# Performance work log

Hardware: AMD Instinct MI355X
Metric: run time of the kernel (lower is better)

The kernel has to match this reference:

```python
import jax, jax.numpy as jnp
import numpy as np

N_NODES = 100000
N_EDGES = 1600000
D_IN = 128
D_OUT = 128


def setup_inputs() -> dict:
    key = jax.random.key(0)
    k1, k2, k3, k4, k5 = jax.random.split(key, 5)
    x = jax.random.normal(k1, (N_NODES, D_IN), dtype=jnp.float32)
    row = jax.random.randint(k2, (N_EDGES,), 0, N_NODES, dtype=jnp.int32)
    col = jax.random.randint(k3, (N_EDGES,), 0, N_NODES, dtype=jnp.int32)
    edge_weight = jax.random.uniform(k4, (N_EDGES,), dtype=jnp.float32)
    stdv = 1.0 / np.sqrt(D_OUT)
    weight = jax.random.uniform(k5, (D_IN, D_OUT), dtype=jnp.float32,
                                minval=-stdv, maxval=stdv)
    return {"x": x, "row": row, "col": col,
            "edge_weight": edge_weight, "weight": weight}


def reference(x, row, col, edge_weight, weight):
    # support = x @ W  -- dense feature transform [N, D_OUT]
    support = jnp.matmul(x, weight)
    # out = adj @ support, adj sparse COO: out[row] += w * support[col]
    messages = edge_weight[:, None] * support[col]  # [E, D_OUT]
    out = jax.ops.segment_sum(messages, row, num_segments=N_NODES)
    return out
```

## Files before the change

kernel.cpp:

```cpp
#include <hip/hip_runtime.h>

#define N_NODES 100000
#define N_EDGES 1600000
#define D 128
#define D4 32

#define BM 128
#define GEMM_BLOCKS ((N_NODES + BM - 1) / BM)
#define BUILD_BLOCKS 256
#define TOTAL_BLOCKS (BUILD_BLOCKS + GEMM_BLOCKS)
#define LDK 136

typedef __attribute__((ext_vector_type(8))) short short8;
typedef __attribute__((ext_vector_type(4))) float floatx4;

__device__ __forceinline__ unsigned short f2bf(float f) {
    unsigned int b = __float_as_uint(f);
    b += 0x7FFFu + ((b >> 16) & 1u);
    return (unsigned short)(b >> 16);
}
__device__ __forceinline__ float bf2f(unsigned short u) {
    return __uint_as_float((unsigned int)u << 16);
}

__global__ __launch_bounds__(256) void w_prep(
    const float* __restrict__ W, unsigned short* __restrict__ wt)
{
    int idx = blockIdx.x * 256 + threadIdx.x;
    int k = idx >> 7, n = idx & 127;
    wt[(size_t)n * D + k] = f2bf(W[idx]);
}

__global__ __launch_bounds__(256, 4) void mega(
    const float* __restrict__ x, const unsigned short* __restrict__ wt,
    unsigned short* __restrict__ sup,
    const int* __restrict__ row, const int* __restrict__ col,
    const float* __restrict__ ew,
    int* __restrict__ head, int4* __restrict__ entries)
{
    __shared__ unsigned short xs[BM * LDK];

    const int tid = threadIdx.x;

    if (blockIdx.x < BUILD_BLOCKS) {
        for (int e = blockIdx.x * 256 + tid; e < N_EDGES; e += BUILD_BLOCKS * 256) {
            int nx = atomicExch(&head[row[e]], e);
            entries[e] = make_int4(nx, col[e], __float_as_int(ew[e]), 0);
        }
        return;
    }

    const int brow = (blockIdx.x - BUILD_BLOCKS) * BM;

    {
        const float4* xv = reinterpret_cast<const float4*>(x);
        #pragma unroll
        for (int i = 0; i < 16; ++i) {
            int idx = tid + i * 256;
            int r = idx >> 5, k4 = idx & 31;
            int gr = brow + r;
            float4 v = (gr < N_NODES) ? xv[(size_t)gr * D4 + k4]
                                      : make_float4(0.f, 0.f, 0.f, 0.f);
            ushort4 p;
            p.x = f2bf(v.x); p.y = f2bf(v.y); p.z = f2bf(v.z); p.w = f2bf(v.w);
            *reinterpret_cast<ushort4*>(&xs[r * LDK + k4 * 4]) = p;
        }
    }
    __syncthreads();

    const int wave = tid >> 6;
    const int lane = tid & 63;
    const int l15  = lane & 15;
    const int lkg  = lane >> 4;

    floatx4 acc[2][8];
    #pragma unroll
    for (int m = 0; m < 2; ++m)
        #pragma unroll
        for (int n = 0; n < 8; ++n) acc[m][n] = (floatx4){0.f, 0.f, 0.f, 0.f};

    const short8* bv = reinterpret_cast<const short8*>(wt);
    const int wrow = wave * 32;
    #pragma unroll
    for (int kk = 0; kk < 4; ++kk) {
        int kb = kk * 32 + lkg * 8;
        short8 a0 = *reinterpret_cast<const short8*>(&xs[(wrow + l15) * LDK + kb]);
        short8 a1 = *reinterpret_cast<const short8*>(&xs[(wrow + 16 + l15) * LDK + kb]);
        #pragma unroll
        for (int n = 0; n < 8; ++n) {
            short8 b = bv[(n * 16 + l15) * 16 + kk * 4 + lkg];
            acc[0][n] = __builtin_amdgcn_mfma_f32_16x16x32_bf16(a0, b, acc[0][n], 0, 0, 0);
            acc[1][n] = __builtin_amdgcn_mfma_f32_16x16x32_bf16(a1, b, acc[1][n], 0, 0, 0);
        }
    }

    const int rbase = brow + wrow + lkg * 4;
    #pragma unroll
    for (int m = 0; m < 2; ++m) {
        #pragma unroll
        for (int r = 0; r < 4; ++r) {
            int grow = rbase + m * 16 + r;
            if (grow < N_NODES) {
                #pragma unroll
                for (int n = 0; n < 8; ++n)
                    sup[(size_t)grow * D + n * 16 + l15] = f2bf(acc[m][n][r]);
            }
        }
    }
}

__global__ __launch_bounds__(256) void gather_list(
    const int* __restrict__ head, const int4* __restrict__ entries,
    const unsigned short* __restrict__ sup, float* __restrict__ out)
{
    const int half = threadIdx.x >> 5;
    const int lane = threadIdx.x & 31;
    const int nb = blockIdx.x * 32 + half * 4;

    float4 a0 = {0.f, 0.f, 0.f, 0.f};
    float4 a1 = a0, a2 = a0, a3 = a0;

    int e0 = head[nb + 0];
    int e1 = head[nb + 1];
    int e2 = head[nb + 2];
    int e3 = head[nb + 3];

    while (e0 >= 0 || e1 >= 0 || e2 >= 0 || e3 >= 0) {
        int4 q0 = entries[e0 >= 0 ? e0 : 0];
        int4 q1 = entries[e1 >= 0 ? e1 : 0];
        int4 q2 = entries[e2 >= 0 ? e2 : 0];
        int4 q3 = entries[e3 >= 0 ? e3 : 0];

        ushort4 s0 = reinterpret_cast<const ushort4*>(sup + (size_t)q0.y * D)[lane];
        ushort4 s1 = reinterpret_cast<const ushort4*>(sup + (size_t)q1.y * D)[lane];
        ushort4 s2 = reinterpret_cast<const ushort4*>(sup + (size_t)q2.y * D)[lane];
        ushort4 s3 = reinterpret_cast<const ushort4*>(sup + (size_t)q3.y * D)[lane];

        float w0 = (e0 >= 0) ? __int_as_float(q0.z) : 0.f;
        float w1 = (e1 >= 0) ? __int_as_float(q1.z) : 0.f;
        float w2 = (e2 >= 0) ? __int_as_float(q2.z) : 0.f;
        float w3 = (e3 >= 0) ? __int_as_float(q3.z) : 0.f;

        a0.x = fmaf(w0, bf2f(s0.x), a0.x); a0.y = fmaf(w0, bf2f(s0.y), a0.y);
        a0.z = fmaf(w0, bf2f(s0.z), a0.z); a0.w = fmaf(w0, bf2f(s0.w), a0.w);
        a1.x = fmaf(w1, bf2f(s1.x), a1.x); a1.y = fmaf(w1, bf2f(s1.y), a1.y);
        a1.z = fmaf(w1, bf2f(s1.z), a1.z); a1.w = fmaf(w1, bf2f(s1.w), a1.w);
        a2.x = fmaf(w2, bf2f(s2.x), a2.x); a2.y = fmaf(w2, bf2f(s2.y), a2.y);
        a2.z = fmaf(w2, bf2f(s2.z), a2.z); a2.w = fmaf(w2, bf2f(s2.w), a2.w);
        a3.x = fmaf(w3, bf2f(s3.x), a3.x); a3.y = fmaf(w3, bf2f(s3.y), a3.y);
        a3.z = fmaf(w3, bf2f(s3.z), a3.z); a3.w = fmaf(w3, bf2f(s3.w), a3.w);

        e0 = (e0 >= 0) ? q0.x : -1;
        e1 = (e1 >= 0) ? q1.x : -1;
        e2 = (e2 >= 0) ? q2.x : -1;
        e3 = (e3 >= 0) ? q3.x : -1;
    }

    float4* ov = reinterpret_cast<float4*>(out);
    ov[(size_t)(nb + 0) * D4 + lane] = a0;
    ov[(size_t)(nb + 1) * D4 + lane] = a1;
    ov[(size_t)(nb + 2) * D4 + lane] = a2;
    ov[(size_t)(nb + 3) * D4 + lane] = a3;
}

__device__ __forceinline__ void fma4(float4& a, float s, const float4& b) {
    a.x = fmaf(s, b.x, a.x);
    a.y = fmaf(s, b.y, a.y);
    a.z = fmaf(s, b.z, a.z);
    a.w = fmaf(s, b.w, a.w);
}

__global__ __launch_bounds__(256) void gemm_xw(
    const float* __restrict__ x, const float* __restrict__ W,
    unsigned short* __restrict__ sup)
{
    __shared__ float4 xs[32 * D4];
    const int tid = threadIdx.x;
    const int block_row = blockIdx.x * 32;

    const float4* xv = reinterpret_cast<const float4*>(x) + (size_t)block_row * D4;
    #pragma unroll
    for (int i = 0; i < 4; ++i) xs[tid + i * 256] = xv[tid + i * 256];
    __syncthreads();

    const int cg = tid & 31;
    const int rg = tid >> 5;
    const float4* Wv = reinterpret_cast<const float4*>(W);

    float4 acc0 = {0.f, 0.f, 0.f, 0.f};
    float4 acc1 = acc0, acc2 = acc0, acc3 = acc0;

    const int r0 = rg * 4;
    #pragma unroll 8
    for (int k4 = 0; k4 < D4; ++k4) {
        float4 xa = xs[(r0 + 0) * D4 + k4];
        float4 xb = xs[(r0 + 1) * D4 + k4];
        float4 xc = xs[(r0 + 2) * D4 + k4];
        float4 xd = xs[(r0 + 3) * D4 + k4];
        float4 w0 = Wv[(k4 * 4 + 0) * D4 + cg];
        fma4(acc0, xa.x, w0); fma4(acc1, xb.x, w0);
        fma4(acc2, xc.x, w0); fma4(acc3, xd.x, w0);
        float4 w1 = Wv[(k4 * 4 + 1) * D4 + cg];
        fma4(acc0, xa.y, w1); fma4(acc1, xb.y, w1);
        fma4(acc2, xc.y, w1); fma4(acc3, xd.y, w1);
        float4 w2 = Wv[(k4 * 4 + 2) * D4 + cg];
        fma4(acc0, xa.z, w2); fma4(acc1, xb.z, w2);
        fma4(acc2, xc.z, w2); fma4(acc3, xd.z, w2);
        float4 w3 = Wv[(k4 * 4 + 3) * D4 + cg];
        fma4(acc0, xa.w, w3); fma4(acc1, xb.w, w3);
        fma4(acc2, xc.w, w3); fma4(acc3, xd.w, w3);
    }

    ushort4 p;
    #define STORE_BF16(ACC, R)                                            \
        p.x = f2bf(ACC.x); p.y = f2bf(ACC.y);                             \
        p.z = f2bf(ACC.z); p.w = f2bf(ACC.w);                             \
        *reinterpret_cast<ushort4*>(sup + (size_t)(block_row + r0 + R) * D + cg * 4) = p;
    STORE_BF16(acc0, 0)
    STORE_BF16(acc1, 1)
    STORE_BF16(acc2, 2)
    STORE_BF16(acc3, 3)
    #undef STORE_BF16
}

__global__ __launch_bounds__(256) void scatter_edges(
    const int* __restrict__ row, const int* __restrict__ col,
    const float* __restrict__ ew, const unsigned short* __restrict__ sup,
    float* __restrict__ out)
{
    const int e = blockIdx.x * 8 + (threadIdx.x >> 5);
    if (e >= N_EDGES) return;
    const int lane = threadIdx.x & 31;

    const int r = row[e];
    const int c = col[e];
    const float w = ew[e];
    ushort4 s = reinterpret_cast<const ushort4*>(sup + (size_t)c * D)[lane];
    float* o = out + (size_t)r * D + lane * 4;
    atomicAdd(o + 0, w * bf2f(s.x));
    atomicAdd(o + 1, w * bf2f(s.y));
    atomicAdd(o + 2, w * bf2f(s.z));
    atomicAdd(o + 3, w * bf2f(s.w));
}

extern "C" void kernel_launch(void* const* d_in, const int* in_sizes, int n_in,
                              void* d_out, int out_size, void* d_ws, size_t ws_size,
                              hipStream_t stream)
{
    const float* x      = (const float*)d_in[0];
    const int*   row    = (const int*)d_in[1];
    const int*   col    = (const int*)d_in[2];
    const float* ew     = (const float*)d_in[3];
    const float* weight = (const float*)d_in[4];
    float* out = (float*)d_out;

    char* ws = (char*)d_ws;
    const size_t off_sup     = 0;
    const size_t off_head    = off_sup + (size_t)N_NODES * D * 2;
    const size_t off_entries = off_head + (((size_t)N_NODES * 4 + 15) & ~(size_t)15);
    const size_t off_wt      = off_entries + (size_t)N_EDGES * 16;
    const size_t required    = off_wt + (size_t)D * D * 2;

    unsigned short* sup = (unsigned short*)(ws + off_sup);

    if (ws_size >= required) {
        int*  head    = (int*)(ws + off_head);
        int4* entries = (int4*)(ws + off_entries);
        unsigned short* wt = (unsigned short*)(ws + off_wt);

        hipMemsetAsync(head, 0xFF, (size_t)N_NODES * 4, stream);
        w_prep<<<D * D / 256, 256, 0, stream>>>(weight, wt);

        mega<<<TOTAL_BLOCKS, 256, 0, stream>>>(
            x, wt, sup, row, col, ew, head, entries);

        gather_list<<<N_NODES / 32, 256, 0, stream>>>(head, entries, sup, out);
    } else {
        gemm_xw<<<N_NODES / 32, 256, 0, stream>>>(x, weight, sup);
        hipMemsetAsync(d_out, 0, (size_t)N_NODES * D * sizeof(float), stream);
        scatter_edges<<<N_EDGES / 8, 256, 0, stream>>>(row, col, ew, sup, out);
    }
}
```

Before: 184.2 us.

## Split each node's edge list into two parity chains and batch list-build loads

Each node now gets two linked-list heads chosen by edge parity, so a node's edges form two chains of half length. The gather walks both chains at once with separate accumulators and sums them, which shortens the serial pointer-chasing dependency per node while keeping four chains in flight per thread. The build loop is unrolled by four so row, col and weight loads are issued ahead of the atomics. In exchange the head array and its memset double in size, and the gather uses twice as many blocks, each covering half as many nodes.

```diff
diff --git a/kernel.cpp b/kernel.cpp
--- a/kernel.cpp
+++ b/kernel.cpp
@@ -43,8 +43,24 @@
     const int tid = threadIdx.x;
 
     if (blockIdx.x < BUILD_BLOCKS) {
-        for (int e = blockIdx.x * 256 + tid; e < N_EDGES; e += BUILD_BLOCKS * 256) {
-            int nx = atomicExch(&head[row[e]], e);
+        const int S = BUILD_BLOCKS * 256;
+        int e = blockIdx.x * 256 + tid;
+        const int par = e & 1;
+        for (; e + 3 * S < N_EDGES; e += 4 * S) {
+            int r0 = row[e], r1 = row[e + S], r2 = row[e + 2 * S], r3 = row[e + 3 * S];
+            int c0 = col[e], c1 = col[e + S], c2 = col[e + 2 * S], c3 = col[e + 3 * S];
+            float w0 = ew[e], w1 = ew[e + S], w2 = ew[e + 2 * S], w3 = ew[e + 3 * S];
+            int n0 = atomicExch(&head[(r0 << 1) | par], e);
+            int n1 = atomicExch(&head[(r1 << 1) | par], e + S);
+            int n2 = atomicExch(&head[(r2 << 1) | par], e + 2 * S);
+            int n3 = atomicExch(&head[(r3 << 1) | par], e + 3 * S);
+            entries[e]         = make_int4(n0, c0, __float_as_int(w0), 0);
+            entries[e + S]     = make_int4(n1, c1, __float_as_int(w1), 0);
+            entries[e + 2 * S] = make_int4(n2, c2, __float_as_int(w2), 0);
+            entries[e + 3 * S] = make_int4(n3, c3, __float_as_int(w3), 0);
+        }
+        for (; e < N_EDGES; e += S) {
+            int nx = atomicExch(&head[(row[e] << 1) | par], e);
             entries[e] = make_int4(nx, col[e], __float_as_int(ew[e]), 0);
         }
         return;
@@ -109,21 +125,21 @@
     }
 }
 
+#define GATHER_BLOCKS (N_NODES / 16)
+
 __global__ __launch_bounds__(256) void gather_list(
     const int* __restrict__ head, const int4* __restrict__ entries,
     const unsigned short* __restrict__ sup, float* __restrict__ out)
 {
     const int half = threadIdx.x >> 5;
     const int lane = threadIdx.x & 31;
-    const int nb = blockIdx.x * 32 + half * 4;
-
-    float4 a0 = {0.f, 0.f, 0.f, 0.f};
-    float4 a1 = a0, a2 = a0, a3 = a0;
-
-    int e0 = head[nb + 0];
-    int e1 = head[nb + 1];
-    int e2 = head[nb + 2];
-    int e3 = head[nb + 3];
+    const int nb = blockIdx.x * 16 + half * 2;
+
+    int4 h = *reinterpret_cast<const int4*>(head + 2 * nb);
+    int e0 = h.x, e1 = h.y, e2 = h.z, e3 = h.w;
+
+    float4 A0 = {0.f, 0.f, 0.f, 0.f};
+    float4 A1 = A0, A2 = A0, A3 = A0;
 
     while (e0 >= 0 || e1 >= 0 || e2 >= 0 || e3 >= 0) {
         int4 q0 = entries[e0 >= 0 ? e0 : 0];
@@ -141,14 +157,14 @@
         float w2 = (e2 >= 0) ? __int_as_float(q2.z) : 0.f;
         float w3 = (e3 >= 0) ? __int_as_float(q3.z) : 0.f;
 
-        a0.x = fmaf(w0, bf2f(s0.x), a0.x); a0.y = fmaf(w0, bf2f(s0.y), a0.y);
-        a0.z = fmaf(w0, bf2f(s0.z), a0.z); a0.w = fmaf(w0, bf2f(s0.w), a0.w);
-        a1.x = fmaf(w1, bf2f(s1.x), a1.x); a1.y = fmaf(w1, bf2f(s1.y), a1.y);
-        a1.z = fmaf(w1, bf2f(s1.z), a1.z); a1.w = fmaf(w1, bf2f(s1.w), a1.w);
-        a2.x = fmaf(w2, bf2f(s2.x), a2.x); a2.y = fmaf(w2, bf2f(s2.y), a2.y);
-        a2.z = fmaf(w2, bf2f(s2.z), a2.z); a2.w = fmaf(w2, bf2f(s2.w), a2.w);
-        a3.x = fmaf(w3, bf2f(s3.x), a3.x); a3.y = fmaf(w3, bf2f(s3.y), a3.y);
-        a3.z = fmaf(w3, bf2f(s3.z), a3.z); a3.w = fmaf(w3, bf2f(s3.w), a3.w);
+        A0.x = fmaf(w0, bf2f(s0.x), A0.x); A0.y = fmaf(w0, bf2f(s0.y), A0.y);
+        A0.z = fmaf(w0, bf2f(s0.z), A0.z); A0.w = fmaf(w0, bf2f(s0.w), A0.w);
+        A1.x = fmaf(w1, bf2f(s1.x), A1.x); A1.y = fmaf(w1, bf2f(s1.y), A1.y);
+        A1.z = fmaf(w1, bf2f(s1.z), A1.z); A1.w = fmaf(w1, bf2f(s1.w), A1.w);
+        A2.x = fmaf(w2, bf2f(s2.x), A2.x); A2.y = fmaf(w2, bf2f(s2.y), A2.y);
+        A2.z = fmaf(w2, bf2f(s2.z), A2.z); A2.w = fmaf(w2, bf2f(s2.w), A2.w);
+        A3.x = fmaf(w3, bf2f(s3.x), A3.x); A3.y = fmaf(w3, bf2f(s3.y), A3.y);
+        A3.z = fmaf(w3, bf2f(s3.z), A3.z); A3.w = fmaf(w3, bf2f(s3.w), A3.w);
 
         e0 = (e0 >= 0) ? q0.x : -1;
         e1 = (e1 >= 0) ? q1.x : -1;
@@ -156,11 +172,13 @@
         e3 = (e3 >= 0) ? q3.x : -1;
     }
 
+    float4 a0, a1;
+    a0.x = A0.x + A1.x; a0.y = A0.y + A1.y; a0.z = A0.z + A1.z; a0.w = A0.w + A1.w;
+    a1.x = A2.x + A3.x; a1.y = A2.y + A3.y; a1.z = A2.z + A3.z; a1.w = A2.w + A3.w;
+
     float4* ov = reinterpret_cast<float4*>(out);
     ov[(size_t)(nb + 0) * D4 + lane] = a0;
     ov[(size_t)(nb + 1) * D4 + lane] = a1;
-    ov[(size_t)(nb + 2) * D4 + lane] = a2;
-    ov[(size_t)(nb + 3) * D4 + lane] = a3;
 }
 
 __device__ __forceinline__ void fma4(float4& a, float s, const float4& b) {
@@ -257,7 +275,7 @@
     char* ws = (char*)d_ws;
     const size_t off_sup     = 0;
     const size_t off_head    = off_sup + (size_t)N_NODES * D * 2;
-    const size_t off_entries = off_head + (((size_t)N_NODES * 4 + 15) & ~(size_t)15);
+    const size_t off_entries = off_head + (((size_t)N_NODES * 8 + 15) & ~(size_t)15);
     const size_t off_wt      = off_entries + (size_t)N_EDGES * 16;
     const size_t required    = off_wt + (size_t)D * D * 2;
 
@@ -268,13 +286,13 @@
         int4* entries = (int4*)(ws + off_entries);
         unsigned short* wt = (unsigned short*)(ws + off_wt);
 
-        hipMemsetAsync(head, 0xFF, (size_t)N_NODES * 4, stream);
+        hipMemsetAsync(head, 0xFF, (size_t)N_NODES * 8, stream);
         w_prep<<<D * D / 256, 256, 0, stream>>>(weight, wt);
 
         mega<<<TOTAL_BLOCKS, 256, 0, stream>>>(
             x, wt, sup, row, col, ew, head, entries);
 
-        gather_list<<<N_NODES / 32, 256, 0, stream>>>(head, entries, sup, out);
+        gather_list<<<GATHER_BLOCKS, 256, 0, stream>>>(head, entries, sup, out);
     } else {
         gemm_xw<<<N_NODES / 32, 256, 0, stream>>>(x, weight, sup);
         hipMemsetAsync(d_out, 0, (size_t)N_NODES * D * sizeof(float), stream);
```

Result: slower. 190.5 us (+3.4%).
